# Performance work log

Hardware: AMD Instinct MI355X
Metric: run time of the kernel (lower is better)

Reference implementation:

```python
import jax, jax.numpy as jnp
import numpy as np

D = 4        # memory depth
K = 64       # number of locations
N = 262144   # number of time units
KAPPA = K + K * K * D


def setup_inputs() -> dict:
    key = jax.random.key(0)
    k_obs, k_beta = jax.random.split(key)
    obs = jax.random.uniform(k_obs, (N, K), dtype=jnp.float32)          # observations (dense stand-in for csr)
    beta = jax.random.uniform(k_beta, (1, KAPPA), dtype=jnp.float32)    # matches uniform_(0, 1) init
    return {"obs": obs, "beta": beta, "d": D}


def reference(obs, beta, d):
    n, k = obs.shape
    beta0 = beta[0, :k]                       # [K] base intensity
    B3 = beta[0, k:].reshape(k, k, d)         # [K, K, d]; B3[k,j,i] multiplies obs[t-d+i, j]
    # sliding windows W[t, i, j] = obs[t + i, j], t = 0..n-d-1  (window ending just before t+d)
    idx = jnp.arange(n - d)[:, None] + jnp.arange(d)[None, :]  # [T', d]
    W = obs[idx]                                               # [T', d, K]
    # lam[t, k] = beta0[k] + sum_{i,j} W[t,i,j] * B3[k,j,i]  (the kron(I_K, vec) matmul collapsed)
    lam = beta0[None, :] + jnp.einsum('tij,kji->tk', W, B3)    # [T', K]
    tgt = obs[d:]                                              # omega_t for t = d..n-1
    loglik = jnp.sum(tgt * jnp.log(lam)) - jnp.sum(lam)
    return loglik, lam
```

## Files before the change

kernel.cpp:

```cpp
#include <hip/hip_runtime.h>
#include <hip/hip_bf16.h>

#define NROWS 262144
#define KO 64
#define DW 4
#define TROWS (NROWS - DW)

using f32x4  = __attribute__((ext_vector_type(4))) float;
using bf16x8 = __attribute__((ext_vector_type(8))) __bf16;

__global__ void pack_b_kernel(const float* __restrict__ beta, __bf16* __restrict__ bpack,
                              float* __restrict__ out0) {
  int idx = blockIdx.x * 256 + threadIdx.x;
  if (idx == 0) out0[0] = 0.f;
  if (idx >= 2048) return;
  int lane = idx & 63;
  int kt = (idx >> 6) & 3;
  int cc = idx >> 8;
  int kout = kt * 16 + (lane & 15);
  int cbase = cc * 32 + 8 * (lane >> 4);
  __bf16* dst = bpack + idx * 8;
#pragma unroll
  for (int e = 0; e < 8; ++e) {
    int c = cbase + e;
    int i = c >> 6;
    int j = c & 63;
    dst[e] = (__bf16)beta[KO + (kout * KO + j) * DW + i];
  }
}

__launch_bounds__(256, 3)
__global__ void poisson_main_kernel(const float* __restrict__ obs,
                                    const float* __restrict__ beta,
                                    const __bf16* __restrict__ bpack,
                                    float* __restrict__ lam_out,
                                    float* __restrict__ loglik) {
  const int wave = threadIdx.x >> 6;
  const int lane = threadIdx.x & 63;
  const int lr = lane & 15;
  const int lg = lane >> 4;
  const int t0 = blockIdx.x * 128 + wave * 32;

  const float* pA[2];
#pragma unroll
  for (int ts = 0; ts < 2; ++ts) {
    int rb = t0 + 16 * ts + lr;
    if (rb > NROWS - 4) rb = NROWS - 4;
    pA[ts] = obs + rb * KO + 8 * lg;
  }
  const __bf16* pB = bpack + lane * 8;

  f32x4 acc[2][4];
#pragma unroll
  for (int ts = 0; ts < 2; ++ts)
#pragma unroll
    for (int kt = 0; kt < 4; ++kt)
      acc[ts][kt] = (f32x4){0.f, 0.f, 0.f, 0.f};

  f32x4 rbuf[2][8];
#define LOADG(BUF, G) do {                                                  \
    _Pragma("unroll")                                                       \
    for (int ccp = 0; ccp < 2; ++ccp)                                       \
      _Pragma("unroll")                                                     \
      for (int ts = 0; ts < 2; ++ts) {                                      \
        const float* p = pA[ts] + (G) * KO + ccp * 32;                      \
        rbuf[BUF][ccp * 4 + ts * 2 + 0] = *reinterpret_cast<const f32x4*>(p);     \
        rbuf[BUF][ccp * 4 + ts * 2 + 1] = *reinterpret_cast<const f32x4*>(p + 4); \
      }                                                                     \
  } while (0)

  LOADG(0, 0);
#pragma unroll
  for (int g = 0; g < 4; ++g) {
    if (g < 3) LOADG((g + 1) & 1, g + 1);
#pragma unroll
    for (int ccp = 0; ccp < 2; ++ccp) {
      const int cc = 2 * g + ccp;
      bf16x8 ax[2];
#pragma unroll
      for (int ts = 0; ts < 2; ++ts) {
        f32x4 f0 = rbuf[g & 1][ccp * 4 + ts * 2 + 0];
        f32x4 f1 = rbuf[g & 1][ccp * 4 + ts * 2 + 1];
        bf16x8 av;
        av[0] = (__bf16)f0[0]; av[1] = (__bf16)f0[1];
        av[2] = (__bf16)f0[2]; av[3] = (__bf16)f0[3];
        av[4] = (__bf16)f1[0]; av[5] = (__bf16)f1[1];
        av[6] = (__bf16)f1[2]; av[7] = (__bf16)f1[3];
        ax[ts] = av;
      }
#pragma unroll
      for (int kt = 0; kt < 4; ++kt) {
        bf16x8 bfrag = *reinterpret_cast<const bf16x8*>(pB + (cc * 4 + kt) * 512);
        acc[0][kt] = __builtin_amdgcn_mfma_f32_16x16x32_bf16(ax[0], bfrag, acc[0][kt], 0, 0, 0);
        acc[1][kt] = __builtin_amdgcn_mfma_f32_16x16x32_bf16(ax[1], bfrag, acc[1][kt], 0, 0, 0);
      }
    }
  }
#undef LOADG

  float b0v[4];
#pragma unroll
  for (int kt = 0; kt < 4; ++kt) b0v[kt] = beta[kt * 16 + lr];

  float part = 0.f;
#pragma unroll
  for (int ts = 0; ts < 2; ++ts)
#pragma unroll
    for (int r = 0; r < 4; ++r) {
      const int t = t0 + 16 * ts + 4 * lg + r;
      if (t < TROWS) {
        float* po = lam_out + t * KO + lr;
        const float* ptg = obs + (t + DW) * KO + lr;
#pragma unroll
        for (int kt = 0; kt < 4; ++kt) {
          const float lam = acc[ts][kt][r] + b0v[kt];
          po[kt * 16] = lam;
          part += ptg[kt * 16] * __logf(lam) - lam;
        }
      }
    }

#pragma unroll
  for (int off = 32; off > 0; off >>= 1)
    part += __shfl_down(part, off, 64);

  __shared__ float wpart[4];
  if (lane == 0) wpart[wave] = part;
  __syncthreads();
  if (threadIdx.x == 0)
    atomicAdd(loglik, wpart[0] + wpart[1] + wpart[2] + wpart[3]);
}

extern "C" void kernel_launch(void* const* d_in, const int* in_sizes, int n_in,
                              void* d_out, int out_size, void* d_ws, size_t ws_size,
                              hipStream_t stream) {
  const float* obs  = (const float*)d_in[0];
  const float* beta = (const float*)d_in[1];
  float* out = (float*)d_out;

  __bf16* bpack = (__bf16*)d_ws;

  hipLaunchKernelGGL(pack_b_kernel, dim3(8), dim3(256), 0, stream, beta, bpack, out);
  hipLaunchKernelGGL(poisson_main_kernel, dim3(2048), dim3(256), 0, stream,
                     obs, beta, bpack, out + 1, out);
}
```

Baseline: 158.2 us.

## Stage obs window rows in swizzled LDS via global_load_lds and reuse for targets

Each block now loads its 136 needed obs rows once into LDS using direct global-to-LDS loads with an XOR swizzle. The A fragments for all four shifted windows and the Poisson target values are read from LDS instead of issuing overlapping global loads per shift. Launch bounds are raised to 4 blocks per CU. The cost is about 34KB of LDS per block, which limits occupancy, plus a full-barrier wait before any MFMA work starts, so loads and compute no longer overlap.

Result: faster. 139.7 us (-11.7%).

```diff
diff --git a/kernel.cpp b/kernel.cpp
--- a/kernel.cpp
+++ b/kernel.cpp
@@ -6,8 +6,14 @@
 #define DW 4
 #define TROWS (NROWS - DW)
 
+#define AROWS 136
+#define ACHUNKS (AROWS * 16)
+
 using f32x4  = __attribute__((ext_vector_type(4))) float;
 using bf16x8 = __attribute__((ext_vector_type(8))) __bf16;
+
+typedef const __attribute__((address_space(1))) void* gas_ptr;
+typedef __attribute__((address_space(3))) void* las_ptr;
 
 __global__ void pack_b_kernel(const float* __restrict__ beta, __bf16* __restrict__ bpack,
                               float* __restrict__ out0) {
@@ -29,26 +35,38 @@
   }
 }
 
-__launch_bounds__(256, 3)
+__launch_bounds__(256, 4)
 __global__ void poisson_main_kernel(const float* __restrict__ obs,
                                     const float* __restrict__ beta,
                                     const __bf16* __restrict__ bpack,
                                     float* __restrict__ lam_out,
                                     float* __restrict__ loglik) {
-  const int wave = threadIdx.x >> 6;
-  const int lane = threadIdx.x & 63;
+  __shared__ float aLds[AROWS * KO];
+  const int tid  = threadIdx.x;
+  const int wave = tid >> 6;
+  const int lane = tid & 63;
   const int lr = lane & 15;
   const int lg = lane >> 4;
-  const int t0 = blockIdx.x * 128 + wave * 32;
+  const int t0 = blockIdx.x * 128;
 
-  const float* pA[2];
 #pragma unroll
-  for (int ts = 0; ts < 2; ++ts) {
-    int rb = t0 + 16 * ts + lr;
-    if (rb > NROWS - 4) rb = NROWS - 4;
-    pA[ts] = obs + rb * KO + 8 * lg;
+  for (int it = 0; it < 9; ++it) {
+    int c = tid + it * 256;
+    if (c < ACHUNKS) {
+      int arow = c >> 4;
+      int cb   = (c & 15) << 4;
+      int row  = t0 + arow;
+      if (row > NROWS - 1) row = NROWS - 1;
+      const float* src = obs + row * KO + ((cb ^ ((arow & 7) << 4)) >> 2);
+      __builtin_amdgcn_global_load_lds((gas_ptr)src,
+          (las_ptr)(aLds + (it * 256 + wave * 64) * 4), 16, 0, 0);
+    }
   }
+
   const __bf16* pB = bpack + lane * 8;
+  float b0v[4];
+#pragma unroll
+  for (int kt = 0; kt < 4; ++kt) b0v[kt] = beta[kt * 16 + lr];
 
   f32x4 acc[2][4];
 #pragma unroll
@@ -57,65 +75,54 @@
     for (int kt = 0; kt < 4; ++kt)
       acc[ts][kt] = (f32x4){0.f, 0.f, 0.f, 0.f};
 
-  f32x4 rbuf[2][8];
-#define LOADG(BUF, G) do {                                                  \
-    _Pragma("unroll")                                                       \
-    for (int ccp = 0; ccp < 2; ++ccp)                                       \
-      _Pragma("unroll")                                                     \
-      for (int ts = 0; ts < 2; ++ts) {                                      \
-        const float* p = pA[ts] + (G) * KO + ccp * 32;                      \
-        rbuf[BUF][ccp * 4 + ts * 2 + 0] = *reinterpret_cast<const f32x4*>(p);     \
-        rbuf[BUF][ccp * 4 + ts * 2 + 1] = *reinterpret_cast<const f32x4*>(p + 4); \
-      }                                                                     \
-  } while (0)
+  asm volatile("s_waitcnt vmcnt(0)" ::: "memory");
+  __syncthreads();
 
-  LOADG(0, 0);
+  const int rowb = 32 * wave + lr;
 #pragma unroll
-  for (int g = 0; g < 4; ++g) {
-    if (g < 3) LOADG((g + 1) & 1, g + 1);
+  for (int cc = 0; cc < 8; ++cc) {
+    const int i  = cc >> 1;
+    const int sw = ((lr + i) & 7) << 4;
+    const int cb = (cc & 1) * 128 + 32 * lg;
+    bf16x8 ax[2];
 #pragma unroll
-    for (int ccp = 0; ccp < 2; ++ccp) {
-      const int cc = 2 * g + ccp;
-      bf16x8 ax[2];
+    for (int ts = 0; ts < 2; ++ts) {
+      const char* base = (const char*)aLds + (rowb + 16 * ts + i) * 256;
+      f32x4 f0 = *reinterpret_cast<const f32x4*>(base + ((cb +  0) ^ sw));
+      f32x4 f1 = *reinterpret_cast<const f32x4*>(base + ((cb + 16) ^ sw));
+      bf16x8 av;
+      av[0] = (__bf16)f0[0]; av[1] = (__bf16)f0[1];
+      av[2] = (__bf16)f0[2]; av[3] = (__bf16)f0[3];
+      av[4] = (__bf16)f1[0]; av[5] = (__bf16)f1[1];
+      av[6] = (__bf16)f1[2]; av[7] = (__bf16)f1[3];
+      ax[ts] = av;
+    }
 #pragma unroll
-      for (int ts = 0; ts < 2; ++ts) {
-        f32x4 f0 = rbuf[g & 1][ccp * 4 + ts * 2 + 0];
-        f32x4 f1 = rbuf[g & 1][ccp * 4 + ts * 2 + 1];
-        bf16x8 av;
-        av[0] = (__bf16)f0[0]; av[1] = (__bf16)f0[1];
-        av[2] = (__bf16)f0[2]; av[3] = (__bf16)f0[3];
-        av[4] = (__bf16)f1[0]; av[5] = (__bf16)f1[1];
-        av[6] = (__bf16)f1[2]; av[7] = (__bf16)f1[3];
-        ax[ts] = av;
-      }
-#pragma unroll
-      for (int kt = 0; kt < 4; ++kt) {
-        bf16x8 bfrag = *reinterpret_cast<const bf16x8*>(pB + (cc * 4 + kt) * 512);
-        acc[0][kt] = __builtin_amdgcn_mfma_f32_16x16x32_bf16(ax[0], bfrag, acc[0][kt], 0, 0, 0);
-        acc[1][kt] = __builtin_amdgcn_mfma_f32_16x16x32_bf16(ax[1], bfrag, acc[1][kt], 0, 0, 0);
-      }
+    for (int kt = 0; kt < 4; ++kt) {
+      bf16x8 bfrag = *reinterpret_cast<const bf16x8*>(pB + (cc * 4 + kt) * 512);
+      acc[0][kt] = __builtin_amdgcn_mfma_f32_16x16x32_bf16(ax[0], bfrag, acc[0][kt], 0, 0, 0);
+      acc[1][kt] = __builtin_amdgcn_mfma_f32_16x16x32_bf16(ax[1], bfrag, acc[1][kt], 0, 0, 0);
     }
   }
-#undef LOADG
-
-  float b0v[4];
-#pragma unroll
-  for (int kt = 0; kt < 4; ++kt) b0v[kt] = beta[kt * 16 + lr];
 
   float part = 0.f;
 #pragma unroll
   for (int ts = 0; ts < 2; ++ts)
 #pragma unroll
     for (int r = 0; r < 4; ++r) {
-      const int t = t0 + 16 * ts + 4 * lg + r;
-      if (t < TROWS) {
-        float* po = lam_out + t * KO + lr;
-        const float* ptg = obs + (t + DW) * KO + lr;
+      const int tl = 32 * wave + 16 * ts + 4 * lg + r;
+      const int tg = t0 + tl;
+      if (tg < TROWS) {
+        const int trow = tl + DW;
+        const int swt  = (trow & 7) << 4;
+        const char* tb = (const char*)aLds + trow * 256;
+        float* po = lam_out + tg * KO + lr;
 #pragma unroll
         for (int kt = 0; kt < 4; ++kt) {
           const float lam = acc[ts][kt][r] + b0v[kt];
           po[kt * 16] = lam;
-          part += ptg[kt * 16] * __logf(lam) - lam;
+          const float tgt = *reinterpret_cast<const float*>(tb + (((kt * 16 + lr) * 4) ^ swt));
+          part += tgt * __logf(lam) - lam;
         }
       }
     }
```
